# Optimization experiments

Measured on AMD Instinct MI355X. Metric: run time of the kernel, lower is better.

## Reference

```python
import jax, jax.numpy as jnp
import numpy as np

B, M, D = 4, 2048, 1024
N, P = 64, 32  # num_experts, slots_per_expert


def setup_inputs() -> dict:
    key = jax.random.key(0)
    k1, k2, k3, k4 = jax.random.split(key, 4)
    x = jax.random.normal(k1, (B, M, D), dtype=jnp.float32)
    phi = jax.random.normal(k2, (D, N, P), dtype=jnp.float32) * (1.0 / np.sqrt(D))
    W = jax.random.normal(k3, (N, D, D), dtype=jnp.float32) * (1.0 / np.sqrt(D))
    b = jax.random.normal(k4, (N, D), dtype=jnp.float32) * 0.01
    return {"x": x, "phi": phi, "W": W, "b": b}


def reference(x, phi, W, b):
    # logits: (b, m, n, p)
    logits = jnp.einsum('bmd,dnp->bmnp', x, phi)
    # dispatch: softmax over dim=0 (batch), faithful to the given source
    dispatch = jax.nn.softmax(logits, axis=0)
    # combine: softmax over flattened (n*p) slot axis
    bsz, m, n, p = logits.shape
    combine = jax.nn.softmax(logits.reshape(bsz, m, n * p), axis=-1).reshape(bsz, m, n, p)
    # slot inputs: (b, n, p, d)
    slots = jnp.einsum('bmd,bmnp->bnpd', x, dispatch)
    # per-expert GEMM + bias
    y = jnp.einsum('bnpd,nde->bnpe', slots, W) + b[None, :, None, :]
    # combine back to tokens: (b, m, d)
    out = jnp.einsum('bnpd,bmnp->bmd', y, combine)
    return out
```

## Files before the change

### kernel.cpp

```cpp
#include <hip/hip_runtime.h>
#include <cstddef>

#define Bb 4
#define Mm 2048
#define Dd 1024
#define Nn 64
#define Pp 32
#define NP 2048
#define BM 8192

typedef __attribute__((ext_vector_type(4))) float v4f;
typedef __attribute__((ext_vector_type(8))) short v8s;

__device__ inline unsigned short f2b(float f) {
  union { float f; unsigned u; } v; v.f = f;
  unsigned r = v.u + 0x7fff + ((v.u >> 16) & 1);
  return (unsigned short)(r >> 16);
}

__device__ inline void gld16(const void* g, void* l) {
  __builtin_amdgcn_global_load_lds(
      (const __attribute__((address_space(1))) unsigned*)g,
      (__attribute__((address_space(3))) unsigned*)l, 16, 0, 0);
}

__global__ __launch_bounds__(256) void k_cvt(const float* __restrict__ in,
                                             unsigned short* __restrict__ out) {
  size_t i = (size_t)blockIdx.x * 256 + threadIdx.x;
  float4 v0 = ((const float4*)in)[2 * i];
  float4 v1 = ((const float4*)in)[2 * i + 1];
  uint4 o;
  o.x = (unsigned)f2b(v0.x) | ((unsigned)f2b(v0.y) << 16);
  o.y = (unsigned)f2b(v0.z) | ((unsigned)f2b(v0.w) << 16);
  o.z = (unsigned)f2b(v1.x) | ((unsigned)f2b(v1.y) << 16);
  o.w = (unsigned)f2b(v1.z) | ((unsigned)f2b(v1.w) << 16);
  *(uint4*)&out[8 * i] = o;
}

__global__ __launch_bounds__(256) void k_tr_f2b(const float* __restrict__ in, size_t sin_,
                                                unsigned short* __restrict__ out, size_t sout,
                                                int R, int C) {
  __shared__ unsigned short t[32][33];
  const int r0 = blockIdx.y * 32, c0 = blockIdx.x * 32;
  const float* ib = in + (size_t)blockIdx.z * sin_;
  unsigned short* ob = out + (size_t)blockIdx.z * sout;
  const int tr = threadIdx.x >> 3;
  const int tc = (threadIdx.x & 7) * 4;
  float4 v = *(const float4*)&ib[(size_t)(r0 + tr) * C + c0 + tc];
  t[tr][tc + 0] = f2b(v.x); t[tr][tc + 1] = f2b(v.y);
  t[tr][tc + 2] = f2b(v.z); t[tr][tc + 3] = f2b(v.w);
  __syncthreads();
  ushort4 o;
  o.x = t[tc + 0][tr]; o.y = t[tc + 1][tr];
  o.z = t[tc + 2][tr]; o.w = t[tc + 3][tr];
  *(ushort4*)&ob[(size_t)(c0 + tr) * R + r0 + tc] = o;
}

__global__ __launch_bounds__(256) void k_tr_b2b(const unsigned short* __restrict__ in, size_t sin_,
                                                unsigned short* __restrict__ out, size_t sout,
                                                int R, int C) {
  __shared__ unsigned short t[32][33];
  const int r0 = blockIdx.y * 32, c0 = blockIdx.x * 32;
  const unsigned short* ib = in + (size_t)blockIdx.z * sin_;
  unsigned short* ob = out + (size_t)blockIdx.z * sout;
  const int tr = threadIdx.x >> 3;
  const int tc = (threadIdx.x & 7) * 4;
  ushort4 v = *(const ushort4*)&ib[(size_t)(r0 + tr) * C + c0 + tc];
  t[tr][tc + 0] = v.x; t[tr][tc + 1] = v.y;
  t[tr][tc + 2] = v.z; t[tr][tc + 3] = v.w;
  __syncthreads();
  ushort4 o;
  o.x = t[tc + 0][tr]; o.y = t[tc + 1][tr];
  o.z = t[tc + 2][tr]; o.w = t[tc + 3][tr];
  *(ushort4*)&ob[(size_t)(c0 + tr) * R + r0 + tc] = o;
}

template <int OUT_BF16>
__global__ __launch_bounds__(256) void k_gemm(const unsigned short* __restrict__ A, size_t sA,
                                              const unsigned short* __restrict__ B, size_t sB,
                                              void* __restrict__ C, size_t sC,
                                              int M, int N, int K) {
  __shared__ unsigned short As[128][32];
  __shared__ unsigned short Bs[128][32];
  const int tid = threadIdx.x;
  const int wv = tid >> 6, ln = tid & 63;
  const int wm = wv & 1, wn = wv >> 1;
  const int row0 = blockIdx.y * 128, col0 = blockIdx.x * 128;
  const unsigned short* Ab = A + (size_t)blockIdx.z * sA + (size_t)row0 * K;
  const unsigned short* Bbp = B + (size_t)blockIdx.z * sB + (size_t)col0 * K;
  const int sr = ln >> 2;
  const int sc = (ln & 3) * 8;
  const int fr = ln & 15, fc = (ln >> 4) * 8;
  v4f acc[4][4];
#pragma unroll
  for (int i = 0; i < 4; ++i)
#pragma unroll
    for (int j = 0; j < 4; ++j) { v4f z = {0.f, 0.f, 0.f, 0.f}; acc[i][j] = z; }

  for (int kt = 0; kt < K; kt += 32) {
    __syncthreads();
    gld16(Ab + (size_t)(32 * wv + sr) * K + kt + sc,      &As[32 * wv][0]);
    gld16(Ab + (size_t)(32 * wv + 16 + sr) * K + kt + sc, &As[32 * wv + 16][0]);
    gld16(Bbp + (size_t)(32 * wv + sr) * K + kt + sc,      &Bs[32 * wv][0]);
    gld16(Bbp + (size_t)(32 * wv + 16 + sr) * K + kt + sc, &Bs[32 * wv + 16][0]);
    __syncthreads();
    v8s a[4], b[4];
#pragma unroll
    for (int i = 0; i < 4; ++i) a[i] = *(const v8s*)&As[64 * wm + 16 * i + fr][fc];
#pragma unroll
    for (int j = 0; j < 4; ++j) b[j] = *(const v8s*)&Bs[64 * wn + 16 * j + fr][fc];
#pragma unroll
    for (int i = 0; i < 4; ++i)
#pragma unroll
      for (int j = 0; j < 4; ++j)
        acc[i][j] = __builtin_amdgcn_mfma_f32_16x16x32_bf16(a[i], b[j], acc[i][j], 0, 0, 0);
  }
  const int er = (ln >> 4) * 4, ec = ln & 15;
#pragma unroll
  for (int i = 0; i < 4; ++i)
#pragma unroll
    for (int j = 0; j < 4; ++j) {
      int r = row0 + 64 * wm + 16 * i + er;
      int c = col0 + 64 * wn + 16 * j + ec;
      if (OUT_BF16) {
        unsigned short* Cp = (unsigned short*)C + (size_t)blockIdx.z * sC + (size_t)r * N + c;
#pragma unroll
        for (int q = 0; q < 4; ++q) Cp[(size_t)q * N] = f2b(acc[i][j][q]);
      } else {
        float* Cp = (float*)C + (size_t)blockIdx.z * sC + (size_t)r * N + c;
#pragma unroll
        for (int q = 0; q < 4; ++q) Cp[(size_t)q * N] = acc[i][j][q];
      }
    }
}

__global__ __launch_bounds__(256) void k_softmax(const float* __restrict__ logits,
                                                 unsigned short* __restrict__ dispatch,
                                                 unsigned short* __restrict__ combine) {
  __shared__ float sh[Bb][NP];
  __shared__ float red[256];
  const int m = blockIdx.x;
  const int tid = threadIdx.x;
#pragma unroll
  for (int b = 0; b < Bb; ++b) {
    const float4* src = (const float4*)(logits + ((size_t)b * Mm + m) * NP);
#pragma unroll
    for (int it = 0; it < 2; ++it) ((float4*)sh[b])[tid + it * 256] = src[tid + it * 256];
  }
  __syncthreads();
#pragma unroll
  for (int it = 0; it < 8; ++it) {
    int np = tid + it * 256;
    float v0 = sh[0][np], v1 = sh[1][np], v2 = sh[2][np], v3 = sh[3][np];
    float mx = fmaxf(fmaxf(v0, v1), fmaxf(v2, v3));
    float e0 = __expf(v0 - mx), e1 = __expf(v1 - mx);
    float e2 = __expf(v2 - mx), e3 = __expf(v3 - mx);
    float inv = 1.0f / (e0 + e1 + e2 + e3);
    dispatch[((size_t)0 * Mm + m) * NP + np] = f2b(e0 * inv);
    dispatch[((size_t)1 * Mm + m) * NP + np] = f2b(e1 * inv);
    dispatch[((size_t)2 * Mm + m) * NP + np] = f2b(e2 * inv);
    dispatch[((size_t)3 * Mm + m) * NP + np] = f2b(e3 * inv);
  }
#pragma unroll
  for (int b = 0; b < Bb; ++b) {
    float lmax = -3.0e38f;
#pragma unroll
    for (int it = 0; it < 8; ++it) lmax = fmaxf(lmax, sh[b][tid + it * 256]);
    red[tid] = lmax;
    __syncthreads();
    for (int s = 128; s > 0; s >>= 1) {
      if (tid < s) red[tid] = fmaxf(red[tid], red[tid + s]);
      __syncthreads();
    }
    float mx = red[0];
    __syncthreads();
    float lsum = 0.0f;
#pragma unroll
    for (int it = 0; it < 8; ++it) lsum += __expf(sh[b][tid + it * 256] - mx);
    red[tid] = lsum;
    __syncthreads();
    for (int s = 128; s > 0; s >>= 1) {
      if (tid < s) red[tid] += red[tid + s];
      __syncthreads();
    }
    float inv = 1.0f / red[0];
    __syncthreads();
#pragma unroll
    for (int it = 0; it < 8; ++it) {
      int np = tid + it * 256;
      combine[((size_t)b * Mm + m) * NP + np] = f2b(__expf(sh[b][np] - mx) * inv);
    }
  }
}

__global__ __launch_bounds__(256) void k_y_mfma(const unsigned short* __restrict__ slots,
                                                const float* __restrict__ W,
                                                const float* __restrict__ bias,
                                                unsigned short* __restrict__ y) {
  __shared__ unsigned short As[128][32];
  __shared__ unsigned short Bs[128][40];
  const int n = blockIdx.z;
  const int col0 = blockIdx.x * 128;
  const int tid = threadIdx.x;
  const int wv = tid >> 6, ln = tid & 63;
  const int wm = wv & 1, wn = wv >> 1;
  const int sr = ln >> 2, sc = (ln & 3) * 8;
  const int fr = ln & 15, fc = (ln >> 4) * 8;
  const float* Wn = W + (size_t)n * Dd * Dd;
  v4f acc[4][4];
#pragma unroll
  for (int i = 0; i < 4; ++i)
#pragma unroll
    for (int j = 0; j < 4; ++j) { v4f z = {0.f, 0.f, 0.f, 0.f}; acc[i][j] = z; }

  const int te = tid & 127;
  const int tks = (tid >> 7) * 4;

  for (int kt = 0; kt < Dd; kt += 32) {
    __syncthreads();
    {
      int r1 = 32 * wv + sr;
      int r2 = r1 + 16;
      size_t g1 = ((size_t)(r1 >> 5) * NP + n * Pp + (r1 & 31)) * Dd;
      size_t g2 = ((size_t)(r2 >> 5) * NP + n * Pp + (r2 & 31)) * Dd;
      gld16(slots + g1 + kt + sc, &As[32 * wv][0]);
      gld16(slots + g2 + kt + sc, &As[32 * wv + 16][0]);
    }
#pragma unroll
    for (int kk = 0; kk < 4; ++kk) {
      int k0 = kk * 8 + tks;
      float f0 = Wn[(size_t)(kt + k0 + 0) * Dd + col0 + te];
      float f1 = Wn[(size_t)(kt + k0 + 1) * Dd + col0 + te];
      float f2 = Wn[(size_t)(kt + k0 + 2) * Dd + col0 + te];
      float f3 = Wn[(size_t)(kt + k0 + 3) * Dd + col0 + te];
      unsigned long long pk = (unsigned long long)f2b(f0) |
                              ((unsigned long long)f2b(f1) << 16) |
                              ((unsigned long long)f2b(f2) << 32) |
                              ((unsigned long long)f2b(f3) << 48);
      *(unsigned long long*)&Bs[te][k0] = pk;
    }
    __syncthreads();
    v8s a[4], b[4];
#pragma unroll
    for (int i = 0; i < 4; ++i) a[i] = *(const v8s*)&As[64 * wm + 16 * i + fr][fc];
#pragma unroll
    for (int j = 0; j < 4; ++j) b[j] = *(const v8s*)&Bs[64 * wn + 16 * j + fr][fc];
#pragma unroll
    for (int i = 0; i < 4; ++i)
#pragma unroll
      for (int j = 0; j < 4; ++j)
        acc[i][j] = __builtin_amdgcn_mfma_f32_16x16x32_bf16(a[i], b[j], acc[i][j], 0, 0, 0);
  }
  const int er = (ln >> 4) * 4, ec = ln & 15;
  float bv[4];
#pragma unroll
  for (int j = 0; j < 4; ++j) bv[j] = bias[(size_t)n * Dd + col0 + 64 * wn + 16 * j + ec];
#pragma unroll
  for (int i = 0; i < 4; ++i)
#pragma unroll
    for (int j = 0; j < 4; ++j) {
      int c = col0 + 64 * wn + 16 * j + ec;
#pragma unroll
      for (int q = 0; q < 4; ++q) {
        int r = 64 * wm + 16 * i + er + q;
        size_t row = (size_t)(r >> 5) * NP + n * Pp + (r & 31);
        y[row * Dd + c] = f2b(acc[i][j][q] + bv[j]);
      }
    }
}

extern "C" void kernel_launch(void* const* d_in, const int* in_sizes, int n_in,
                              void* d_out, int out_size, void* d_ws, size_t ws_size,
                              hipStream_t stream) {
  const float* x    = (const float*)d_in[0];
  const float* phi  = (const float*)d_in[1];
  const float* W    = (const float*)d_in[2];
  const float* bias = (const float*)d_in[3];
  float* out = (float*)d_out;
  char* ws = (char*)d_ws;

  float*          logits = (float*)(ws);
  unsigned short* dispT  = (unsigned short*)(ws);
  unsigned short* slots  = (unsigned short*)(ws + 33554432);
  unsigned short* y_b    = (unsigned short*)(ws);
  unsigned short* yT     = (unsigned short*)(ws + 16777216);
  unsigned short* disp_b = (unsigned short*)(ws + 67108864);
  unsigned short* comb_b = (unsigned short*)(ws + 100663296);
  unsigned short* xb     = (unsigned short*)(ws + 134217728);
  unsigned short* xT     = (unsigned short*)(ws + 134217728);
  unsigned short* phiT   = (unsigned short*)(ws + 150994944);

  k_cvt<<<4096, 256, 0, stream>>>(x, xb);
  k_tr_f2b<<<dim3(64, 32, 1), 256, 0, stream>>>(phi, 0, phiT, 0, Dd, NP);
  k_gemm<0><<<dim3(16, 64, 1), 256, 0, stream>>>(xb, 0, phiT, 0, logits, 0, BM, NP, Dd);
  k_tr_f2b<<<dim3(32, 64, Bb), 256, 0, stream>>>(x, (size_t)Mm * Dd, xT, (size_t)Dd * Mm, Mm, Dd);
  k_softmax<<<Mm, 256, 0, stream>>>(logits, disp_b, comb_b);
  k_tr_b2b<<<dim3(64, 64, Bb), 256, 0, stream>>>(disp_b, (size_t)Mm * NP, dispT, (size_t)NP * Mm, Mm, NP);
  k_gemm<1><<<dim3(8, 16, Bb), 256, 0, stream>>>(dispT, (size_t)NP * Mm, xT, (size_t)Dd * Mm,
                                                 slots, (size_t)NP * Dd, NP, Dd, Mm);
  k_y_mfma<<<dim3(8, 1, Nn), 256, 0, stream>>>(slots, W, bias, y_b);
  k_tr_b2b<<<dim3(32, 64, Bb), 256, 0, stream>>>(y_b, (size_t)NP * Dd, yT, (size_t)Dd * NP, NP, Dd);
  k_gemm<0><<<dim3(8, 16, Bb), 256, 0, stream>>>(comb_b, (size_t)Mm * NP, yT, (size_t)Dd * NP,
                                                 out, (size_t)Mm * Dd, Mm, Dd, NP);
}
```

Before: 629.4 us.

## Fuse x conversion and transpose, warp-shuffle softmax reductions, vectorize W staging

Merges the x-to-bf16 conversion and the x transpose into one kernel, so x is read from global memory once and both layouts are written from the same tile. Replaces the shared-memory tree reductions in the combine softmax with wavefront shuffle reductions, which cuts the number of block barriers. In the expert GEMM, W is now loaded with float4 reads and packed into LDS as bf16 pairs instead of scalar strided loads. The workspace buffers are laid out without overlap so xb and xT can coexist, at the cost of a larger workspace footprint.

```diff
diff --git a/kernel.cpp b/kernel.cpp
--- a/kernel.cpp
+++ b/kernel.cpp
@@ -1,4 +1,5 @@
 #include <hip/hip_runtime.h>
+#include <hip/hip_bf16.h>
 #include <cstddef>
 
 #define Bb 4
@@ -24,36 +25,44 @@
       (__attribute__((address_space(3))) unsigned*)l, 16, 0, 0);
 }
 
-__global__ __launch_bounds__(256) void k_cvt(const float* __restrict__ in,
-                                             unsigned short* __restrict__ out) {
-  size_t i = (size_t)blockIdx.x * 256 + threadIdx.x;
-  float4 v0 = ((const float4*)in)[2 * i];
-  float4 v1 = ((const float4*)in)[2 * i + 1];
-  uint4 o;
-  o.x = (unsigned)f2b(v0.x) | ((unsigned)f2b(v0.y) << 16);
-  o.y = (unsigned)f2b(v0.z) | ((unsigned)f2b(v0.w) << 16);
-  o.z = (unsigned)f2b(v1.x) | ((unsigned)f2b(v1.y) << 16);
-  o.w = (unsigned)f2b(v1.z) | ((unsigned)f2b(v1.w) << 16);
-  *(uint4*)&out[8 * i] = o;
-}
-
-__global__ __launch_bounds__(256) void k_tr_f2b(const float* __restrict__ in, size_t sin_,
-                                                unsigned short* __restrict__ out, size_t sout,
+__global__ __launch_bounds__(256) void k_xprep(const float* __restrict__ x,
+                                               unsigned short* __restrict__ xb,
+                                               unsigned short* __restrict__ xT) {
+  __shared__ unsigned short t[32][33];
+  const int b = blockIdx.z;
+  const int r0 = blockIdx.y * 32;
+  const int c0 = blockIdx.x * 32;
+  const float* ib = x + (size_t)b * Mm * Dd;
+  const int tr = threadIdx.x >> 3;
+  const int tc = (threadIdx.x & 7) * 4;
+  float4 v = *(const float4*)&ib[(size_t)(r0 + tr) * Dd + c0 + tc];
+  ushort4 s;
+  s.x = f2b(v.x); s.y = f2b(v.y); s.z = f2b(v.z); s.w = f2b(v.w);
+  *(ushort4*)&xb[(size_t)b * Mm * Dd + (size_t)(r0 + tr) * Dd + c0 + tc] = s;
+  t[tr][tc + 0] = s.x; t[tr][tc + 1] = s.y;
+  t[tr][tc + 2] = s.z; t[tr][tc + 3] = s.w;
+  __syncthreads();
+  ushort4 o;
+  o.x = t[tc + 0][tr]; o.y = t[tc + 1][tr];
+  o.z = t[tc + 2][tr]; o.w = t[tc + 3][tr];
+  *(ushort4*)&xT[(size_t)b * Dd * Mm + (size_t)(c0 + tr) * Mm + r0 + tc] = o;
+}
+
+__global__ __launch_bounds__(256) void k_tr_f2b(const float* __restrict__ in,
+                                                unsigned short* __restrict__ out,
                                                 int R, int C) {
   __shared__ unsigned short t[32][33];
   const int r0 = blockIdx.y * 32, c0 = blockIdx.x * 32;
-  const float* ib = in + (size_t)blockIdx.z * sin_;
-  unsigned short* ob = out + (size_t)blockIdx.z * sout;
   const int tr = threadIdx.x >> 3;
   const int tc = (threadIdx.x & 7) * 4;
-  float4 v = *(const float4*)&ib[(size_t)(r0 + tr) * C + c0 + tc];
+  float4 v = *(const float4*)&in[(size_t)(r0 + tr) * C + c0 + tc];
   t[tr][tc + 0] = f2b(v.x); t[tr][tc + 1] = f2b(v.y);
   t[tr][tc + 2] = f2b(v.z); t[tr][tc + 3] = f2b(v.w);
   __syncthreads();
   ushort4 o;
   o.x = t[tc + 0][tr]; o.y = t[tc + 1][tr];
   o.z = t[tc + 2][tr]; o.w = t[tc + 3][tr];
-  *(ushort4*)&ob[(size_t)(c0 + tr) * R + r0 + tc] = o;
+  *(ushort4*)&out[(size_t)(c0 + tr) * R + r0 + tc] = o;
 }
 
 __global__ __launch_bounds__(256) void k_tr_b2b(const unsigned short* __restrict__ in, size_t sin_,
@@ -138,9 +147,11 @@
                                                  unsigned short* __restrict__ dispatch,
                                                  unsigned short* __restrict__ combine) {
   __shared__ float sh[Bb][NP];
-  __shared__ float red[256];
+  __shared__ float redm[Bb][4];
+  __shared__ float reds[Bb][4];
   const int m = blockIdx.x;
   const int tid = threadIdx.x;
+  const int wv = tid >> 6, ln = tid & 63;
 #pragma unroll
   for (int b = 0; b < Bb; ++b) {
     const float4* src = (const float4*)(logits + ((size_t)b * Mm + m) * NP);
@@ -166,25 +177,19 @@
     float lmax = -3.0e38f;
 #pragma unroll
     for (int it = 0; it < 8; ++it) lmax = fmaxf(lmax, sh[b][tid + it * 256]);
-    red[tid] = lmax;
-    __syncthreads();
-    for (int s = 128; s > 0; s >>= 1) {
-      if (tid < s) red[tid] = fmaxf(red[tid], red[tid + s]);
-      __syncthreads();
-    }
-    float mx = red[0];
-    __syncthreads();
+#pragma unroll
+    for (int o = 32; o > 0; o >>= 1) lmax = fmaxf(lmax, __shfl_xor(lmax, o, 64));
+    if (ln == 0) redm[b][wv] = lmax;
+    __syncthreads();
+    float mx = fmaxf(fmaxf(redm[b][0], redm[b][1]), fmaxf(redm[b][2], redm[b][3]));
     float lsum = 0.0f;
 #pragma unroll
     for (int it = 0; it < 8; ++it) lsum += __expf(sh[b][tid + it * 256] - mx);
-    red[tid] = lsum;
-    __syncthreads();
-    for (int s = 128; s > 0; s >>= 1) {
-      if (tid < s) red[tid] += red[tid + s];
-      __syncthreads();
-    }
-    float inv = 1.0f / red[0];
-    __syncthreads();
+#pragma unroll
+    for (int o = 32; o > 0; o >>= 1) lsum += __shfl_xor(lsum, o, 64);
+    if (ln == 0) reds[b][wv] = lsum;
+    __syncthreads();
+    float inv = 1.0f / (reds[b][0] + reds[b][1] + reds[b][2] + reds[b][3]);
 #pragma unroll
     for (int it = 0; it < 8; ++it) {
       int np = tid + it * 256;
@@ -213,9 +218,6 @@
 #pragma unroll
     for (int j = 0; j < 4; ++j) { v4f z = {0.f, 0.f, 0.f, 0.f}; acc[i][j] = z; }
 
-  const int te = tid & 127;
-  const int tks = (tid >> 7) * 4;
-
   for (int kt = 0; kt < Dd; kt += 32) {
     __syncthreads();
     {
@@ -227,17 +229,17 @@
       gld16(slots + g2 + kt + sc, &As[32 * wv + 16][0]);
     }
 #pragma unroll
-    for (int kk = 0; kk < 4; ++kk) {
-      int k0 = kk * 8 + tks;
-      float f0 = Wn[(size_t)(kt + k0 + 0) * Dd + col0 + te];
-      float f1 = Wn[(size_t)(kt + k0 + 1) * Dd + col0 + te];
-      float f2 = Wn[(size_t)(kt + k0 + 2) * Dd + col0 + te];
-      float f3 = Wn[(size_t)(kt + k0 + 3) * Dd + col0 + te];
-      unsigned long long pk = (unsigned long long)f2b(f0) |
-                              ((unsigned long long)f2b(f1) << 16) |
-                              ((unsigned long long)f2b(f2) << 32) |
-                              ((unsigned long long)f2b(f3) << 48);
-      *(unsigned long long*)&Bs[te][k0] = pk;
+    for (int it = 0; it < 2; ++it) {
+      int idx = tid + it * 256;
+      int k = (idx >> 5) * 2;
+      int eseg = (idx & 31) * 4;
+      const float* wp = &Wn[(size_t)(kt + k) * Dd + col0 + eseg];
+      float4 r0 = *(const float4*)wp;
+      float4 r1 = *(const float4*)(wp + Dd);
+      *(__hip_bfloat162*)&Bs[eseg + 0][k] = __float22bfloat162_rn(float2{r0.x, r1.x});
+      *(__hip_bfloat162*)&Bs[eseg + 1][k] = __float22bfloat162_rn(float2{r0.y, r1.y});
+      *(__hip_bfloat162*)&Bs[eseg + 2][k] = __float22bfloat162_rn(float2{r0.z, r1.z});
+      *(__hip_bfloat162*)&Bs[eseg + 3][k] = __float22bfloat162_rn(float2{r0.w, r1.w});
     }
     __syncthreads();
     v8s a[4], b[4];
@@ -280,20 +282,19 @@
   char* ws = (char*)d_ws;
 
   float*          logits = (float*)(ws);
-  unsigned short* dispT  = (unsigned short*)(ws);
-  unsigned short* slots  = (unsigned short*)(ws + 33554432);
-  unsigned short* y_b    = (unsigned short*)(ws);
-  unsigned short* yT     = (unsigned short*)(ws + 16777216);
   unsigned short* disp_b = (unsigned short*)(ws + 67108864);
   unsigned short* comb_b = (unsigned short*)(ws + 100663296);
-  unsigned short* xb     = (unsigned short*)(ws + 134217728);
-  unsigned short* xT     = (unsigned short*)(ws + 134217728);
-  unsigned short* phiT   = (unsigned short*)(ws + 150994944);
-
-  k_cvt<<<4096, 256, 0, stream>>>(x, xb);
-  k_tr_f2b<<<dim3(64, 32, 1), 256, 0, stream>>>(phi, 0, phiT, 0, Dd, NP);
+  unsigned short* dispT  = (unsigned short*)(ws + 134217728);
+  unsigned short* xb     = (unsigned short*)(ws + 167772160);
+  unsigned short* xT     = (unsigned short*)(ws + 184549376);
+  unsigned short* phiT   = (unsigned short*)(ws + 201326592);
+  unsigned short* slots  = (unsigned short*)(ws + 209715200);
+  unsigned short* y_b    = (unsigned short*)(ws + 226492416);
+  unsigned short* yT     = (unsigned short*)(ws + 243269632);
+
+  k_xprep<<<dim3(32, 64, Bb), 256, 0, stream>>>(x, xb, xT);
+  k_tr_f2b<<<dim3(64, 32, 1), 256, 0, stream>>>(phi, phiT, Dd, NP);
   k_gemm<0><<<dim3(16, 64, 1), 256, 0, stream>>>(xb, 0, phiT, 0, logits, 0, BM, NP, Dd);
-  k_tr_f2b<<<dim3(32, 64, Bb), 256, 0, stream>>>(x, (size_t)Mm * Dd, xT, (size_t)Dd * Mm, Mm, Dd);
   k_softmax<<<Mm, 256, 0, stream>>>(logits, disp_b, comb_b);
   k_tr_b2b<<<dim3(64, 64, Bb), 256, 0, stream>>>(disp_b, (size_t)Mm * NP, dispT, (size_t)NP * Mm, Mm, NP);
   k_gemm<1><<<dim3(8, 16, Bb), 256, 0, stream>>>(dispT, (size_t)NP * Mm, xT, (size_t)Dd * Mm,
```

Result: no change. 627.2 us (-0.4%).
